# Optimization experiments

Measured on AMD Instinct MI355X. Metric: run time of the kernel, lower is better.

Reference implementation:

```python
import jax, jax.numpy as jnp
import numpy as np

N_NODES = 50000
N_EDGES = 200000
D_IN = 512
D_OUT = 512

def setup_inputs() -> dict:
    key = jax.random.key(0)
    k1, k2, k3, k4, k5, k6 = jax.random.split(key, 6)
    h = jax.random.normal(k1, (N_NODES, D_IN), dtype=jnp.float32)
    W = jax.random.normal(k2, (D_IN, D_OUT), dtype=jnp.float32) * (1.0 / np.sqrt(D_IN))
    b = jax.random.normal(k3, (D_OUT,), dtype=jnp.float32) * 0.01
    edge_weight = jax.random.uniform(k4, (N_EDGES,), dtype=jnp.float32)
    src = jax.random.randint(k5, (N_EDGES,), 0, N_NODES, dtype=jnp.int32)
    dst = jax.random.randint(k6, (N_EDGES,), 0, N_NODES, dtype=jnp.int32)
    return {"h": h, "W": W, "b": b, "edge_weight": edge_weight, "src": src, "dst": dst}

def reference(h, W, b, edge_weight, src, dst):
    # Linear projection of source-node features (nn.Linear)
    h_proj = h @ W + b                                   # [N, D_OUT]
    # u_mul_e: gather projected src features, scale by scalar edge weight
    msg = h_proj[src] * edge_weight[:, None]             # [E, D_OUT]
    # mean aggregation over incoming edges per destination node (DGL fn.mean)
    sums = jax.ops.segment_sum(msg, dst, num_segments=N_NODES)          # [N, D_OUT]
    cnt = jax.ops.segment_sum(jnp.ones_like(edge_weight), dst, num_segments=N_NODES)  # [N]
    agg = sums / jnp.maximum(cnt, 1.0)[:, None]          # zero-in-degree nodes -> 0
    # ReLU then dropout (eval mode -> identity)
    return jax.nn.relu(agg)
```

## Files before the change

kernel.cpp:

```cpp
#include <hip/hip_runtime.h>

#define NNODES 50000
#define NEDGES 200000
#define DDIM 512

typedef __attribute__((ext_vector_type(8))) short bf16x8;
typedef __attribute__((ext_vector_type(4))) float f32x4;

static __device__ __forceinline__ unsigned short f2bf(float f) {
  unsigned u = __float_as_uint(f);
  unsigned r = (u + 0x7fffu + ((u >> 16) & 1u)) >> 16;
  return (unsigned short)r;
}

static __device__ __forceinline__ void gload_lds16(const void* g, void* l) {
  __builtin_amdgcn_global_load_lds(
      (const __attribute__((address_space(1))) unsigned int*)g,
      (__attribute__((address_space(3))) unsigned int*)l, 16, 0, 0);
}

static __device__ __forceinline__ bf16x8 cvt_frag(f32x4 lo, f32x4 hi) {
  union { bf16x8 v; unsigned u[4]; } r;
  asm("v_cvt_pk_bf16_f32 %0, %1, %2" : "=v"(r.u[0]) : "v"(lo.x), "v"(lo.y));
  asm("v_cvt_pk_bf16_f32 %0, %1, %2" : "=v"(r.u[1]) : "v"(lo.z), "v"(lo.w));
  asm("v_cvt_pk_bf16_f32 %0, %1, %2" : "=v"(r.u[2]) : "v"(hi.x), "v"(hi.y));
  asm("v_cvt_pk_bf16_f32 %0, %1, %2" : "=v"(r.u[3]) : "v"(hi.z), "v"(hi.w));
  return r.v;
}

__global__ __launch_bounds__(256) void cvt_wt_kernel(
    const float* __restrict__ W, unsigned short* __restrict__ Wt,
    int* __restrict__ deg) {
  const int gid = (blockIdx.x + blockIdx.y * gridDim.x) * 256 + threadIdx.x;
  if (gid < NNODES) deg[gid] = 0;

  __shared__ float t[32][33];
  const int n0 = blockIdx.x * 32, k0 = blockIdx.y * 32;
  const int tx = threadIdx.x & 31, ty = threadIdx.x >> 5;
  for (int r = ty; r < 32; r += 8)
    t[r][tx] = W[(size_t)(k0 + r) * DDIM + n0 + tx];
  __syncthreads();
  for (int r = ty; r < 32; r += 8)
    Wt[(size_t)(n0 + r) * DDIM + k0 + tx] = f2bf(t[tx][r]);
}

__global__ __launch_bounds__(256) void gemm_mfma_kernel(
    const float* __restrict__ A, const unsigned short* __restrict__ Bt,
    const float* __restrict__ bias, unsigned short* __restrict__ C, int M) {
  __shared__ float Af[2][128 * 32];
  __shared__ unsigned short Bs[2][128 * 32];
  const int tid = threadIdx.x;
  const int wid = tid >> 6, lane = tid & 63;

  const int nwg = gridDim.x;
  const int q = nwg >> 3, rr = nwg & 7;
  const int x = blockIdx.x & 7, idx = blockIdx.x >> 3;
  const int wg = x * q + min(x, rr) + idx;

  const int mt = wg >> 2, nt = wg & 3;
  const int bm = mt * 128, bn = nt * 128;
  const int wr = wid >> 1, wc = wid & 1;

  f32x4 acc[4][4] = {};

  const int lr = lane >> 3;
  const int kqs = (lane & 7) ^ lr;
  const int ar0 = min(bm + 0 * 32 + wid * 8 + lr, M - 1);
  const int ar1 = min(bm + 1 * 32 + wid * 8 + lr, M - 1);
  const int ar2 = min(bm + 2 * 32 + wid * 8 + lr, M - 1);
  const int ar3 = min(bm + 3 * 32 + wid * 8 + lr, M - 1);
  const float* pa0 = A + (size_t)ar0 * DDIM + kqs * 4;
  const float* pa1 = A + (size_t)ar1 * DDIM + kqs * 4;
  const float* pa2 = A + (size_t)ar2 * DDIM + kqs * 4;
  const float* pa3 = A + (size_t)ar3 * DDIM + kqs * 4;

  const int r0 = tid >> 2;
  const int cge = (tid & 3) ^ ((r0 >> 1) & 3);
  const unsigned short* b0 = Bt + (size_t)(bn + r0) * DDIM + cge * 8;
  const unsigned short* b1 = Bt + (size_t)(bn + r0 + 64) * DDIM + cge * 8;

  const int l16 = lane & 15, lk = lane >> 4;
  const int lke = lk ^ ((l16 >> 1) & 3);
  const int s7 = l16 & 7;

  const int sOff0 = (wid * 64) * 8;
  const int sOff1 = (256 + wid * 64) * 8;

#define STAGE(buf, k0)                                   \
  do {                                                   \
    gload_lds16(pa0 + (k0), &Af[buf][wid * 256]);        \
    gload_lds16(pa1 + (k0), &Af[buf][1024 + wid * 256]); \
    gload_lds16(pa2 + (k0), &Af[buf][2048 + wid * 256]); \
    gload_lds16(pa3 + (k0), &Af[buf][3072 + wid * 256]); \
    gload_lds16(b0 + (k0), &Bs[buf][sOff0]);             \
    gload_lds16(b1 + (k0), &Bs[buf][sOff1]);             \
  } while (0)

#define COMPUTE(buf)                                                          \
  do {                                                                        \
    bf16x8 af[4], bfr[4];                                                     \
    _Pragma("unroll") for (int i = 0; i < 4; ++i) {                           \
      const int rowi = (wr * 64 + i * 16 + l16) * 32;                         \
      const f32x4 lo = *(const f32x4*)&Af[buf][rowi + (((2 * lk) ^ s7) << 2)];\
      const f32x4 hi = *(const f32x4*)&Af[buf][rowi + (((2 * lk + 1) ^ s7) << 2)]; \
      af[i] = cvt_frag(lo, hi);                                               \
      bfr[i] = *(const bf16x8*)&Bs[buf][(wc * 64 + i * 16 + l16) * 32 + lke * 8]; \
    }                                                                         \
    _Pragma("unroll") for (int i = 0; i < 4; ++i)                             \
        _Pragma("unroll") for (int j = 0; j < 4; ++j)                         \
            acc[i][j] = __builtin_amdgcn_mfma_f32_16x16x32_bf16(              \
                af[i], bfr[j], acc[i][j], 0, 0, 0);                           \
  } while (0)

  STAGE(0, 0);
  __syncthreads();
#pragma unroll 2
  for (int t = 0; t < 15; ++t) {
    const int cur = t & 1;
    STAGE(cur ^ 1, (t + 1) * 32);
    COMPUTE(cur);
    __syncthreads();
  }
  COMPUTE(1);
  __syncthreads();

  unsigned short* cl = (unsigned short*)&Af[0][0] + wid * 4096;
#pragma unroll
  for (int j = 0; j < 4; ++j) {
    const float bv = bias[bn + wc * 64 + j * 16 + l16];
#pragma unroll
    for (int i = 0; i < 4; ++i)
#pragma unroll
      for (int qq = 0; qq < 4; ++qq)
        cl[(i * 16 + lk * 4 + qq) * 64 + j * 16 + l16] =
            f2bf(acc[i][j][qq] + bv);
  }
  __syncthreads();
#pragma unroll
  for (int pass = 0; pass < 8; ++pass) {
    const int rt = pass * 8 + (lane >> 3);
    const int c0 = (lane & 7) * 8;
    const int grow = bm + wr * 64 + rt;
    if (grow < M) {
      const uint4 v = *(const uint4*)&cl[rt * 64 + c0];
      *(uint4*)&C[(size_t)grow * DDIM + bn + wc * 64 + c0] = v;
    }
  }
#undef STAGE
#undef COMPUTE
}

__global__ __launch_bounds__(256) void hist_kernel(const int* __restrict__ dst,
                                                   int* __restrict__ deg, int E) {
  const int e = blockIdx.x * 256 + threadIdx.x;
  if (e < E) atomicAdd(&deg[dst[e]], 1);
}

__global__ __launch_bounds__(256) void chunk_sum_kernel(
    const int* __restrict__ deg, int* __restrict__ part, int n) {
  const int base = blockIdx.x * 1024;
  int v = 0;
  for (int i = threadIdx.x; i < 1024; i += 256) {
    const int idx = base + i;
    v += (idx < n) ? deg[idx] : 0;
  }
#pragma unroll
  for (int s = 32; s; s >>= 1) v += __shfl_down(v, s, 64);
  __shared__ int ws[4];
  if ((threadIdx.x & 63) == 0) ws[threadIdx.x >> 6] = v;
  __syncthreads();
  if (threadIdx.x == 0) part[blockIdx.x] = ws[0] + ws[1] + ws[2] + ws[3];
}

__global__ void scan_part_kernel(int* __restrict__ part, int nb) {
  const int lane = threadIdx.x & 63;
  int v = (lane < nb) ? part[lane] : 0;
  int incl = v;
#pragma unroll
  for (int s = 1; s < 64; s <<= 1) {
    int t = __shfl_up(incl, s, 64);
    if (lane >= s) incl += t;
  }
  if (lane < nb) part[lane] = incl - v;
}

__global__ __launch_bounds__(1024) void chunk_scan_kernel(
    const int* __restrict__ deg, const int* __restrict__ part,
    int* __restrict__ off, int* __restrict__ cur, int n) {
  __shared__ int wsum[16];
  const int tid = threadIdx.x, lane = tid & 63, wid = tid >> 6;
  const int i = blockIdx.x * 1024 + tid;
  const int v = (i < n) ? deg[i] : 0;
  int incl = v;
#pragma unroll
  for (int s = 1; s < 64; s <<= 1) {
    int t = __shfl_up(incl, s, 64);
    if (lane >= s) incl += t;
  }
  if (lane == 63) wsum[wid] = incl;
  __syncthreads();
  if (wid == 0 && lane < 16) {
    int wv = wsum[lane];
#pragma unroll
    for (int s = 1; s < 16; s <<= 1) {
      int t = __shfl_up(wv, s, 16);
      if (lane >= s) wv += t;
    }
    wsum[lane] = wv;
  }
  __syncthreads();
  const int add = part[blockIdx.x] + ((wid > 0) ? wsum[wid - 1] : 0);
  if (i < n) {
    off[i + 1] = add + incl;
    cur[i] = add + incl - v;
  }
  if (i == 0) off[0] = 0;
}

__global__ __launch_bounds__(256) void fill_kernel(
    const int* __restrict__ src, const int* __restrict__ dst,
    const float* __restrict__ ew, int* __restrict__ cur,
    uint2* __restrict__ epair, int E) {
  const int e = blockIdx.x * 256 + threadIdx.x;
  if (e >= E) return;
  const int p = atomicAdd(&cur[dst[e]], 1);
  epair[p] = make_uint2((unsigned)src[e], __float_as_uint(ew[e]));
}

__global__ __launch_bounds__(256) void gather_kernel(
    const unsigned short* __restrict__ hp, const int* __restrict__ off,
    const uint2* __restrict__ epair, float* __restrict__ out, int n) {
  const int node = blockIdx.x * 4 + (threadIdx.x >> 6);
  if (node >= n) return;
  const int lane = threadIdx.x & 63;
  const int beg = off[node], end = off[node + 1];

  float acc[8] = {0.f, 0.f, 0.f, 0.f, 0.f, 0.f, 0.f, 0.f};
  int p = beg;
  for (; p + 2 <= end; p += 2) {
    const uint2 e0 = epair[p];
    const uint2 e1 = epair[p + 1];
    const float w0 = __uint_as_float(e0.y);
    const float w1 = __uint_as_float(e1.y);
    const uint4 u0 = *(const uint4*)(hp + (size_t)e0.x * DDIM + lane * 8);
    const uint4 u1 = *(const uint4*)(hp + (size_t)e1.x * DDIM + lane * 8);
    const unsigned a0[4] = {u0.x, u0.y, u0.z, u0.w};
    const unsigned a1[4] = {u1.x, u1.y, u1.z, u1.w};
#pragma unroll
    for (int qv = 0; qv < 4; ++qv) {
      acc[2 * qv + 0] += w0 * __uint_as_float(a0[qv] << 16) +
                         w1 * __uint_as_float(a1[qv] << 16);
      acc[2 * qv + 1] += w0 * __uint_as_float(a0[qv] & 0xffff0000u) +
                         w1 * __uint_as_float(a1[qv] & 0xffff0000u);
    }
  }
  if (p < end) {
    const uint2 e0 = epair[p];
    const float w0 = __uint_as_float(e0.y);
    const uint4 u0 = *(const uint4*)(hp + (size_t)e0.x * DDIM + lane * 8);
    const unsigned a0[4] = {u0.x, u0.y, u0.z, u0.w};
#pragma unroll
    for (int qv = 0; qv < 4; ++qv) {
      acc[2 * qv + 0] += w0 * __uint_as_float(a0[qv] << 16);
      acc[2 * qv + 1] += w0 * __uint_as_float(a0[qv] & 0xffff0000u);
    }
  }

  const float inv = 1.0f / fmaxf((float)(end - beg), 1.0f);
  f32x4 o0, o1;
  o0.x = fmaxf(acc[0] * inv, 0.f);
  o0.y = fmaxf(acc[1] * inv, 0.f);
  o0.z = fmaxf(acc[2] * inv, 0.f);
  o0.w = fmaxf(acc[3] * inv, 0.f);
  o1.x = fmaxf(acc[4] * inv, 0.f);
  o1.y = fmaxf(acc[5] * inv, 0.f);
  o1.z = fmaxf(acc[6] * inv, 0.f);
  o1.w = fmaxf(acc[7] * inv, 0.f);
  float* orow = out + (size_t)node * DDIM + lane * 8;
  __builtin_nontemporal_store(o0, (f32x4*)(orow + 0));
  __builtin_nontemporal_store(o1, (f32x4*)(orow + 4));
}

extern "C" void kernel_launch(void* const* d_in, const int* in_sizes, int n_in,
                              void* d_out, int out_size, void* d_ws, size_t ws_size,
                              hipStream_t stream) {
  const float* h  = (const float*)d_in[0];
  const float* W  = (const float*)d_in[1];
  const float* b  = (const float*)d_in[2];
  const float* ew = (const float*)d_in[3];
  const int* src  = (const int*)d_in[4];
  const int* dst  = (const int*)d_in[5];
  float* out = (float*)d_out;

  char* ws = (char*)d_ws;
  size_t o = 0;
  auto alloc = [&](size_t bytes) {
    char* p = ws + o;
    o += (bytes + 255) & ~(size_t)255;
    return p;
  };
  unsigned short* hp = (unsigned short*)alloc((size_t)NNODES * DDIM * 2);
  unsigned short* Wt = (unsigned short*)alloc((size_t)DDIM * DDIM * 2);
  int* deg    = (int*)alloc((size_t)NNODES * 4);
  int* off    = (int*)alloc((size_t)(NNODES + 1) * 4);
  int* cur    = (int*)alloc((size_t)NNODES * 4);
  uint2* epair = (uint2*)alloc((size_t)NEDGES * 8);
  int* part   = (int*)alloc(64 * 4);

  const int nchunks = (NNODES + 1023) / 1024;

  dim3 wgrid(16, 16);
  cvt_wt_kernel<<<wgrid, 256, 0, stream>>>(W, Wt, deg);

  const int mtiles = (NNODES + 127) / 128;
  gemm_mfma_kernel<<<mtiles * 4, 256, 0, stream>>>(h, Wt, b, hp, NNODES);

  hist_kernel<<<(NEDGES + 255) / 256, 256, 0, stream>>>(dst, deg, NEDGES);
  chunk_sum_kernel<<<nchunks, 256, 0, stream>>>(deg, part, NNODES);
  scan_part_kernel<<<1, 64, 0, stream>>>(part, nchunks);
  chunk_scan_kernel<<<nchunks, 1024, 0, stream>>>(deg, part, off, cur, NNODES);
  fill_kernel<<<(NEDGES + 255) / 256, 256, 0, stream>>>(src, dst, ew, cur,
                                                        epair, NEDGES);

  gather_kernel<<<(NNODES + 3) / 4, 256, 0, stream>>>(hp, off, epair, out,
                                                      NNODES);
}
```

Measured before the change: 138.0 us.

## Load GEMM A tile straight to registers instead of staging through LDS

The fp32 A operand is now loaded directly from global memory into registers in the MFMA fragment layout and converted to bf16 there, replacing the global_load_lds staging of A and its LDS reads. LDS holds only the B tile plus a dedicated epilogue buffer, which cuts LDS traffic and footprint. In exchange each wave reads its own A rows, so the two waves sharing an M range load the same data twice from global/L2, and 8 extra f32x4 registers per thread stay live across compute, which adds register pressure.

```diff
diff --git a/kernel.cpp b/kernel.cpp
--- a/kernel.cpp
+++ b/kernel.cpp
@@ -47,8 +47,8 @@
 __global__ __launch_bounds__(256) void gemm_mfma_kernel(
     const float* __restrict__ A, const unsigned short* __restrict__ Bt,
     const float* __restrict__ bias, unsigned short* __restrict__ C, int M) {
-  __shared__ float Af[2][128 * 32];
   __shared__ unsigned short Bs[2][128 * 32];
+  __shared__ unsigned short Cl[4][64 * 64];
   const int tid = threadIdx.x;
   const int wid = tid >> 6, lane = tid & 63;
 
@@ -63,68 +63,76 @@
 
   f32x4 acc[4][4] = {};
 
-  const int lr = lane >> 3;
-  const int kqs = (lane & 7) ^ lr;
-  const int ar0 = min(bm + 0 * 32 + wid * 8 + lr, M - 1);
-  const int ar1 = min(bm + 1 * 32 + wid * 8 + lr, M - 1);
-  const int ar2 = min(bm + 2 * 32 + wid * 8 + lr, M - 1);
-  const int ar3 = min(bm + 3 * 32 + wid * 8 + lr, M - 1);
-  const float* pa0 = A + (size_t)ar0 * DDIM + kqs * 4;
-  const float* pa1 = A + (size_t)ar1 * DDIM + kqs * 4;
-  const float* pa2 = A + (size_t)ar2 * DDIM + kqs * 4;
-  const float* pa3 = A + (size_t)ar3 * DDIM + kqs * 4;
+  const int l16 = lane & 15, lk = lane >> 4;
+  const int lke = lk ^ ((l16 >> 1) & 3);
+
+  const float* pA0 = A + (size_t)min(bm + wr * 64 + 0 * 16 + l16, M - 1) * DDIM + lk * 8;
+  const float* pA1 = A + (size_t)min(bm + wr * 64 + 1 * 16 + l16, M - 1) * DDIM + lk * 8;
+  const float* pA2 = A + (size_t)min(bm + wr * 64 + 2 * 16 + l16, M - 1) * DDIM + lk * 8;
+  const float* pA3 = A + (size_t)min(bm + wr * 64 + 3 * 16 + l16, M - 1) * DDIM + lk * 8;
 
   const int r0 = tid >> 2;
   const int cge = (tid & 3) ^ ((r0 >> 1) & 3);
   const unsigned short* b0 = Bt + (size_t)(bn + r0) * DDIM + cge * 8;
   const unsigned short* b1 = Bt + (size_t)(bn + r0 + 64) * DDIM + cge * 8;
-
-  const int l16 = lane & 15, lk = lane >> 4;
-  const int lke = lk ^ ((l16 >> 1) & 3);
-  const int s7 = l16 & 7;
-
   const int sOff0 = (wid * 64) * 8;
   const int sOff1 = (256 + wid * 64) * 8;
 
-#define STAGE(buf, k0)                                   \
-  do {                                                   \
-    gload_lds16(pa0 + (k0), &Af[buf][wid * 256]);        \
-    gload_lds16(pa1 + (k0), &Af[buf][1024 + wid * 256]); \
-    gload_lds16(pa2 + (k0), &Af[buf][2048 + wid * 256]); \
-    gload_lds16(pa3 + (k0), &Af[buf][3072 + wid * 256]); \
-    gload_lds16(b0 + (k0), &Bs[buf][sOff0]);             \
-    gload_lds16(b1 + (k0), &Bs[buf][sOff1]);             \
+  f32x4 t0[4], t1[4];
+  bf16x8 af[4];
+
+#define ALOAD(kf)                            \
+  do {                                       \
+    t0[0] = *(const f32x4*)(pA0 + (kf));     \
+    t1[0] = *(const f32x4*)(pA0 + (kf) + 4); \
+    t0[1] = *(const f32x4*)(pA1 + (kf));     \
+    t1[1] = *(const f32x4*)(pA1 + (kf) + 4); \
+    t0[2] = *(const f32x4*)(pA2 + (kf));     \
+    t1[2] = *(const f32x4*)(pA2 + (kf) + 4); \
+    t0[3] = *(const f32x4*)(pA3 + (kf));     \
+    t1[3] = *(const f32x4*)(pA3 + (kf) + 4); \
+  } while (0)
+
+#define ACVT()                                                               \
+  do {                                                                      \
+    _Pragma("unroll") for (int i = 0; i < 4; ++i) af[i] = cvt_frag(t0[i], t1[i]); \
+  } while (0)
+
+#define BSTAGE(buf, k0)                       \
+  do {                                        \
+    gload_lds16(b0 + (k0), &Bs[buf][sOff0]);  \
+    gload_lds16(b1 + (k0), &Bs[buf][sOff1]);  \
   } while (0)
 
 #define COMPUTE(buf)                                                          \
   do {                                                                        \
-    bf16x8 af[4], bfr[4];                                                     \
-    _Pragma("unroll") for (int i = 0; i < 4; ++i) {                           \
-      const int rowi = (wr * 64 + i * 16 + l16) * 32;                         \
-      const f32x4 lo = *(const f32x4*)&Af[buf][rowi + (((2 * lk) ^ s7) << 2)];\
-      const f32x4 hi = *(const f32x4*)&Af[buf][rowi + (((2 * lk + 1) ^ s7) << 2)]; \
-      af[i] = cvt_frag(lo, hi);                                               \
+    bf16x8 bfr[4];                                                            \
+    _Pragma("unroll") for (int i = 0; i < 4; ++i)                             \
       bfr[i] = *(const bf16x8*)&Bs[buf][(wc * 64 + i * 16 + l16) * 32 + lke * 8]; \
-    }                                                                         \
     _Pragma("unroll") for (int i = 0; i < 4; ++i)                             \
         _Pragma("unroll") for (int j = 0; j < 4; ++j)                         \
             acc[i][j] = __builtin_amdgcn_mfma_f32_16x16x32_bf16(              \
                 af[i], bfr[j], acc[i][j], 0, 0, 0);                           \
   } while (0)
 
-  STAGE(0, 0);
-  __syncthreads();
+  ALOAD(0);
+  BSTAGE(0, 0);
+  ACVT();
+  __syncthreads();
+
 #pragma unroll 2
   for (int t = 0; t < 15; ++t) {
     const int cur = t & 1;
-    STAGE(cur ^ 1, (t + 1) * 32);
+    ALOAD((t + 1) * 32);
+    BSTAGE(cur ^ 1, (t + 1) * 32);
     COMPUTE(cur);
+    ACVT();
     __syncthreads();
   }
   COMPUTE(1);
   __syncthreads();
 
-  unsigned short* cl = (unsigned short*)&Af[0][0] + wid * 4096;
+  unsigned short* cl = &Cl[wid][0];
 #pragma unroll
   for (int j = 0; j < 4; ++j) {
     const float bv = bias[bn + wc * 64 + j * 16 + l16];
@@ -146,7 +154,9 @@
       *(uint4*)&C[(size_t)grow * DDIM + bn + wc * 64 + c0] = v;
     }
   }
-#undef STAGE
+#undef ALOAD
+#undef ACVT
+#undef BSTAGE
 #undef COMPUTE
 }
 
```

New measurement: 203.4 us. 47.4% more time.
